# Kernel tuning notes

Hardware: AMD Instinct MI355X
Metric: run time of the kernel (lower is better)

Reference implementation:

```python
import jax, jax.numpy as jnp
import numpy as np

N = 100000   # nodes
E = 3200000  # directed edges
IN = 128     # in_channels
H = 16       # hidden_channels
OUT = 2      # out_channels
EPS = 1e-5   # BatchNorm eps


def setup_inputs() -> dict:
    key = jax.random.key(0)
    ks = jax.random.split(key, 16)
    x = jax.random.normal(ks[0], (N, IN), jnp.float32)
    edge_index = jax.random.randint(ks[1], (2, E), 0, N, jnp.int32)

    def lin(k, fan_in, fan_out):
        return jax.random.normal(k, (fan_in, fan_out), jnp.float32) / np.sqrt(fan_in)

    return {
        "x": x,
        "edge_index": edge_index,
        "W1": lin(ks[2], IN, H), "b1": jnp.zeros((H,), jnp.float32),
        "W2": lin(ks[3], H, H), "b2": jnp.zeros((H,), jnp.float32),
        "W3": lin(ks[4], H, H), "b3": jnp.zeros((H,), jnp.float32),
        "gamma1": jnp.ones((H,), jnp.float32), "beta1": jnp.zeros((H,), jnp.float32),
        "gamma2": jnp.ones((H,), jnp.float32), "beta2": jnp.zeros((H,), jnp.float32),
        "Wfc": lin(ks[5], H, OUT), "bfc": jnp.zeros((OUT,), jnp.float32),
    }


def reference(x, edge_index, W1, b1, W2, b2, W3, b3,
              gamma1, beta1, gamma2, beta2, Wfc, bfc):
    src, dst = edge_index[0], edge_index[1]
    # symmetric GCN normalization with self loops: deg includes +1 self loop
    deg = jax.ops.segment_sum(jnp.ones((E,), x.dtype), dst, num_segments=N) + 1.0
    dis = jax.lax.rsqrt(deg)                      # [N]
    norm = dis[src] * dis[dst]                    # [E]

    def gcn_conv(h, W, b):
        hw = h @ W                                # [N, F] dense transform
        msg = norm[:, None] * hw[src]             # gather + scale  [E, F]
        agg = jax.ops.segment_sum(msg, dst, num_segments=N)
        agg = agg + (dis * dis)[:, None] * hw     # self-loop contribution
        return agg + b

    def batch_norm(h, g, be):
        mu = h.mean(axis=0)
        var = h.var(axis=0)
        return (h - mu) * jax.lax.rsqrt(var + EPS) * g + be

    h = batch_norm(jax.nn.relu(gcn_conv(x, W1, b1)), gamma1, beta1)
    # dropout is identity in inference / deterministic reference
    h = batch_norm(jax.nn.relu(gcn_conv(h, W2, b2)), gamma2, beta2)
    h = gcn_conv(h, W3, b3)
    return jax.nn.log_softmax(h @ Wfc + bfc, axis=1)
```

## Files before the change

### kernel.cpp

```cpp
#include <hip/hip_runtime.h>
#include <hip/hip_fp16.h>

#define NN 100000
#define EE 3200000
#define INC 128
#define HC 16
#define BN_EPS 1e-5f

#define NPB 256
#define NBUCK ((NN + NPB - 1) / NPB)
#define CAPU 13440
#define BINSZ ((size_t)(NBUCK + 1) * CAPU)
#define BTILE 4096
#define BGRID ((EE + BTILE - 1) / BTILE)
#define SB_CAP 8960
#define GX32 (NN / 32)
#define GGRID (NN / 8)

#define XSTR 132

__device__ __forceinline__ __half2 bits_to_h2(int v) { __half2 h; *(int*)&h = v; return h; }
__device__ __forceinline__ int h2_to_bits(__half2 h) { return *(int*)&h; }


__global__ void init_all(int* __restrict__ bcursor, float* __restrict__ stats,
                         __half2* __restrict__ hws2) {
    int t = threadIdx.x;
    if (t < NBUCK) bcursor[t] = t * CAPU;
    if (t < 64) stats[t] = 0.f;
    if (t < 8) hws2[(size_t)NN * 8 + t] = __half2(__float2half2_rn(0.f));
}


__global__ __launch_bounds__(512) void build_gemm(const int* __restrict__ src,
                          const int* __restrict__ dst,
                          int* __restrict__ bcursor, unsigned* __restrict__ bin,
                          const float* __restrict__ x, const float* __restrict__ W1,
                          __half2* __restrict__ hw_raw) {
    __shared__ __align__(16) char smem[29312];
    int tid = threadIdx.x;
    if (blockIdx.x >= BGRID) {
        float* Ws = (float*)smem;
        float* xs = (float*)(smem + 8192);
        for (int i = tid; i < INC * HC; i += 512) Ws[i] = W1[i];
        int node0 = (blockIdx.x - BGRID) * 32;
        const float4* xsrc = (const float4*)(x + (size_t)node0 * INC);
        float4* xdst = (float4*)xs;
        for (int i = tid; i < 1024; i += 512) {
            int nl = i >> 5, k4 = i & 31;
            xdst[nl * 33 + k4] = xsrc[i];
        }
        __syncthreads();
        int c = tid & 15;
        int nl = tid >> 4;
        int node = node0 + nl;
        const float* xr = xs + nl * XSTR;
        float sum = 0.f;
#pragma unroll
        for (int k = 0; k < INC; ++k) sum += xr[k] * Ws[k * 16 + c];
        float other = __shfl_xor(sum, 1);
        if ((c & 1) == 0) hw_raw[node * 8 + (c >> 1)] = __floats2half2_rn(sum, other);
        return;
    }
    unsigned* stage = (unsigned*)smem;
    unsigned short* sbuck = (unsigned short*)(smem + 16384);
    int* hist  = (int*)(smem + 24576);
    int* loff  = (int*)(smem + 24576 + 1568);
    int* gbase = (int*)(smem + 24576 + 3136);
    int* wsum  = (int*)(smem + 24576 + 4704);
    int lane = tid & 63, wid = tid >> 6;
    for (int k = tid; k < NBUCK; k += 512) hist[k] = 0;
    __syncthreads();
    int e0 = blockIdx.x * BTILE;
    int cnt = min(BTILE, EE - e0);
    int n4 = cnt >> 2;
    const int4* d4 = (const int4*)(dst + e0);
    const int4* s4 = (const int4*)(src + e0);
    int4 dv0 = {0,0,0,0}, dv1 = {0,0,0,0}, sv0 = {0,0,0,0}, sv1 = {0,0,0,0};
    bool va0 = tid < n4, va1 = tid + 512 < n4;
    if (va0) {
        dv0 = d4[tid]; sv0 = s4[tid];
        atomicAdd(&hist[dv0.x >> 8], 1);
        atomicAdd(&hist[dv0.y >> 8], 1);
        atomicAdd(&hist[dv0.z >> 8], 1);
        atomicAdd(&hist[dv0.w >> 8], 1);
    }
    if (va1) {
        dv1 = d4[tid + 512]; sv1 = s4[tid + 512];
        atomicAdd(&hist[dv1.x >> 8], 1);
        atomicAdd(&hist[dv1.y >> 8], 1);
        atomicAdd(&hist[dv1.z >> 8], 1);
        atomicAdd(&hist[dv1.w >> 8], 1);
    }
    __syncthreads();
    int hv = (tid < NBUCK) ? hist[tid] : 0;
    int v = hv;
#pragma unroll
    for (int off = 1; off < 64; off <<= 1) {
        int t = __shfl_up(v, off);
        if (lane >= off) v += t;
    }
    if (lane == 63) wsum[wid] = v;
    __syncthreads();
    if (tid == 0) {
        int run = 0;
#pragma unroll
        for (int j = 0; j < 8; ++j) { int t = wsum[j]; wsum[j] = run; run += t; }
    }
    __syncthreads();
    int excl = v - hv + wsum[wid];
    if (tid < NBUCK) {
        loff[tid] = excl;
        if (hv) gbase[tid] = atomicAdd(&bcursor[tid], hv);
        hist[tid] = 0;
    }
    __syncthreads();
    {
        int d, s, k, p;
        if (va0) {
            d = dv0.x; s = sv0.x; k = d >> 8; p = loff[k] + atomicAdd(&hist[k], 1);
            stage[p] = ((unsigned)(d & 255) << 24) | (unsigned)s; sbuck[p] = (unsigned short)k;
            d = dv0.y; s = sv0.y; k = d >> 8; p = loff[k] + atomicAdd(&hist[k], 1);
            stage[p] = ((unsigned)(d & 255) << 24) | (unsigned)s; sbuck[p] = (unsigned short)k;
            d = dv0.z; s = sv0.z; k = d >> 8; p = loff[k] + atomicAdd(&hist[k], 1);
            stage[p] = ((unsigned)(d & 255) << 24) | (unsigned)s; sbuck[p] = (unsigned short)k;
            d = dv0.w; s = sv0.w; k = d >> 8; p = loff[k] + atomicAdd(&hist[k], 1);
            stage[p] = ((unsigned)(d & 255) << 24) | (unsigned)s; sbuck[p] = (unsigned short)k;
        }
        if (va1) {
            d = dv1.x; s = sv1.x; k = d >> 8; p = loff[k] + atomicAdd(&hist[k], 1);
            stage[p] = ((unsigned)(d & 255) << 24) | (unsigned)s; sbuck[p] = (unsigned short)k;
            d = dv1.y; s = sv1.y; k = d >> 8; p = loff[k] + atomicAdd(&hist[k], 1);
            stage[p] = ((unsigned)(d & 255) << 24) | (unsigned)s; sbuck[p] = (unsigned short)k;
            d = dv1.z; s = sv1.z; k = d >> 8; p = loff[k] + atomicAdd(&hist[k], 1);
            stage[p] = ((unsigned)(d & 255) << 24) | (unsigned)s; sbuck[p] = (unsigned short)k;
            d = dv1.w; s = sv1.w; k = d >> 8; p = loff[k] + atomicAdd(&hist[k], 1);
            stage[p] = ((unsigned)(d & 255) << 24) | (unsigned)s; sbuck[p] = (unsigned short)k;
        }
    }
    __syncthreads();
    for (int i = tid; i < cnt; i += 512) {
        int k = sbuck[i];
        int idx = gbase[k] + (i - loff[k]);
        if (idx < k * CAPU + SB_CAP) bin[idx] = stage[i];
    }
}


__global__ __launch_bounds__(512) void sort_bucket(const int* __restrict__ bcursor,
                            unsigned* __restrict__ bin,
                            unsigned* __restrict__ rowpack, float* __restrict__ dis,
                            const __half2* __restrict__ hw_raw, __half2* __restrict__ hws2) {
    __shared__ unsigned stg[SB_CAP];
    __shared__ int cnt[NPB], pos[NPB], sc[NPB];
    __shared__ int ptot_tot;
    int tid = threadIdx.x;
    for (int k = tid; k < NPB; k += 512) cnt[k] = 0;
    __syncthreads();
    int b = blockIdx.x;
    int beg = b * CAPU;
    int n = min(bcursor[b] - beg, SB_CAP);
    for (int i = tid; i < n; i += 512) {
        unsigned u = bin[beg + i];
        stg[i] = u;
        atomicAdd(&cnt[u >> 24], 1);
    }
    __syncthreads();
    int node = b * NPB + tid;
    int tot = 0, ptot = 0;
    if (tid < NPB) {
        tot = cnt[tid] + ((node < NN) ? 1 : 0);
        ptot = ((tot + 47) / 48) * 48;
        sc[tid] = ptot;
    }
    __syncthreads();
    for (int off = 1; off < NPB; off <<= 1) {
        int t = 0;
        if (tid < NPB && tid >= off) t = sc[tid - off];
        __syncthreads();
        if (tid < NPB) sc[tid] += t;
        __syncthreads();
    }
    int lo = 0;
    if (tid < NPB) {
        lo = sc[tid] - ptot;
        pos[tid] = lo + ((node < NN) ? 1 : 0);
        if (tid == NPB - 1) ptot_tot = sc[tid];
        if (node < NN) {
            rowpack[node] = ((unsigned)min(tot, 511) << 23) | (unsigned)(beg + lo);
            float dv = rsqrtf((float)tot);
            dis[node] = dv;
            __half2 d2 = __float2half2_rn(dv);
            const int4* hr = (const int4*)(hw_raw + (size_t)node * 8);
            int4 a = hr[0], bq = hr[1];
            __half2* ha = (__half2*)&a; __half2* hb = (__half2*)&bq;
#pragma unroll
            for (int j = 0; j < 4; ++j) { ha[j] = __hmul2(ha[j], d2); hb[j] = __hmul2(hb[j], d2); }
            int4* hw = (int4*)(hws2 + (size_t)node * 8);
            hw[0] = a; hw[1] = bq;
        }
    }
    __syncthreads();
    unsigned padv = (unsigned)NN << 5;
    int fillN = ptot_tot;
    for (int i = tid; i < fillN; i += 512) bin[beg + i] = padv;
    __syncthreads();
    if (tid < NPB && node < NN) bin[beg + lo] = (unsigned)node << 5;
    for (int i = tid; i < n; i += 512) {
        unsigned u = stg[i];
        int nl = u >> 24;
        int p = atomicAdd(&pos[nl], 1);
        bin[beg + p] = (u & 0xFFFFFFu) << 5;
    }
}


__global__ void gemm_bn_h_w(const float* __restrict__ agg, const float* __restrict__ stats,
                            const float* __restrict__ gamma, const float* __restrict__ beta,
                            const float* __restrict__ W, const float* __restrict__ dis,
                            __half2* __restrict__ hws2) {
    __shared__ float Ws[HC * HC];
    __shared__ float sc[HC], sf[HC];
    int tid = threadIdx.x;
    if (tid < HC * HC) Ws[tid] = W[tid];
    if (tid < HC) {
        const float invN = 1.0f / NN;
        float mu = stats[tid] * invN;
        float var = stats[16 + tid] * invN - mu * mu;
        float rs = rsqrtf(var + BN_EPS);
        sc[tid] = gamma[tid] * rs;
        sf[tid] = beta[tid] - mu * gamma[tid] * rs;
    }
    __syncthreads();
    int i = blockIdx.x * 256 + tid;
    if (i >= NN * HC) return;
    int n = i >> 4, c = i & 15;
    const float4* ar = (const float4*)(agg + n * HC);
    float sum = 0.f;
#pragma unroll
    for (int q = 0; q < 4; ++q) {
        float4 v = ar[q];
        int k = q * 4;
        float h0 = v.x * sc[k + 0] + sf[k + 0];
        float h1 = v.y * sc[k + 1] + sf[k + 1];
        float h2 = v.z * sc[k + 2] + sf[k + 2];
        float h3 = v.w * sc[k + 3] + sf[k + 3];
        sum += h0 * Ws[(k + 0) * 16 + c] + h1 * Ws[(k + 1) * 16 + c]
             + h2 * Ws[(k + 2) * 16 + c] + h3 * Ws[(k + 3) * 16 + c];
    }
    sum *= dis[n];
    float other = __shfl_xor(sum, 1);
    if ((c & 1) == 0) hws2[n * 8 + (c >> 1)] = __floats2half2_rn(sum, other);
}


__global__ __launch_bounds__(512) void gcn_gather(const unsigned* __restrict__ rowpack,
                           const unsigned* __restrict__ bin,
                           const __half2* __restrict__ hws2,
                           const float* __restrict__ b, float* __restrict__ agg,
                           float* __restrict__ partials) {
    __shared__ float acc[32];
    int tid = threadIdx.x;
    if (tid < 32) acc[tid] = 0.f;
    __syncthreads();
    int lane = tid & 63;
    int node = blockIdx.x * 8 + (tid >> 6);
    int cq = lane & 3;
    int slot = lane >> 2;
    unsigned rp = rowpack[node];
    int beg = (int)(rp & 0x7FFFFFu);
    int tot = (int)(rp >> 23);
    const char* hbase = (const char*)hws2;
    int e0 = beg + slot;
    unsigned v0 = bin[e0], v1 = bin[e0 + 16], v2 = bin[e0 + 32];
    int2 h0 = *(const int2*)(hbase + (size_t)v0 + cq * 8);
    int2 h1 = *(const int2*)(hbase + (size_t)v1 + cq * 8);
    int2 h2 = *(const int2*)(hbase + (size_t)v2 + cq * 8);
    __half2 accA = __hadd2(__hadd2(bits_to_h2(h0.x), bits_to_h2(h1.x)), bits_to_h2(h2.x));
    __half2 accB = __hadd2(__hadd2(bits_to_h2(h0.y), bits_to_h2(h1.y)), bits_to_h2(h2.y));
    for (int off = 48; off < tot; off += 48) {
        unsigned w0 = bin[e0 + off], w1 = bin[e0 + off + 16], w2 = bin[e0 + off + 32];
        int2 g0 = *(const int2*)(hbase + (size_t)w0 + cq * 8);
        int2 g1 = *(const int2*)(hbase + (size_t)w1 + cq * 8);
        int2 g2 = *(const int2*)(hbase + (size_t)w2 + cq * 8);
        accA = __hadd2(accA, __hadd2(__hadd2(bits_to_h2(g0.x), bits_to_h2(g1.x)), bits_to_h2(g2.x)));
        accB = __hadd2(accB, __hadd2(__hadd2(bits_to_h2(g0.y), bits_to_h2(g1.y)), bits_to_h2(g2.y)));
    }
    int ia = h2_to_bits(accA), ib = h2_to_bits(accB);
#pragma unroll
    for (int d = 4; d < 64; d <<= 1) {
        int oa = __shfl_xor(ia, d), ob = __shfl_xor(ib, d);
        accA = __hadd2(accA, bits_to_h2(oa));
        accB = __hadd2(accB, bits_to_h2(ob));
        ia = h2_to_bits(accA); ib = h2_to_bits(accB);
    }
    if (slot == 0) {
        float d = rsqrtf((float)tot);
        float2 sa = __half22float2(accA), sb = __half22float2(accB);
        float t0 = fmaxf(d * sa.x + b[4 * cq + 0], 0.f);
        float t1 = fmaxf(d * sa.y + b[4 * cq + 1], 0.f);
        float t2 = fmaxf(d * sb.x + b[4 * cq + 2], 0.f);
        float t3 = fmaxf(d * sb.y + b[4 * cq + 3], 0.f);
        float4 r; r.x = t0; r.y = t1; r.z = t2; r.w = t3;
        ((float4*)agg)[node * 4 + cq] = r;
        atomicAdd(&acc[4 * cq + 0], t0);
        atomicAdd(&acc[4 * cq + 1], t1);
        atomicAdd(&acc[4 * cq + 2], t2);
        atomicAdd(&acc[4 * cq + 3], t3);
        atomicAdd(&acc[16 + 4 * cq + 0], t0 * t0);
        atomicAdd(&acc[16 + 4 * cq + 1], t1 * t1);
        atomicAdd(&acc[16 + 4 * cq + 2], t2 * t2);
        atomicAdd(&acc[16 + 4 * cq + 3], t3 * t3);
    }
    __syncthreads();
    if (tid < 32) partials[(size_t)blockIdx.x * 32 + tid] = acc[tid];
}


__global__ void reduce_stats(const float* __restrict__ partials, float* __restrict__ stats) {
    int tid = threadIdx.x;
    const int total = GGRID * 32;
    float a = 0.f;
    int i0 = blockIdx.x * 256 + tid;
    for (int i = i0; i < total; i += gridDim.x * 256) a += partials[i];
    __shared__ float acc[32];
    if (tid < 32) acc[tid] = 0.f;
    __syncthreads();
    atomicAdd(&acc[i0 & 31], a);
    __syncthreads();
    if (tid < 32) atomicAdd(&stats[tid], acc[tid]);
}


__global__ __launch_bounds__(512) void gather_fc(const unsigned* __restrict__ rowpack,
                          const unsigned* __restrict__ bin,
                          const __half2* __restrict__ hws2,
                          const float* __restrict__ b, const float* __restrict__ Wfc,
                          const float* __restrict__ bfc, float* __restrict__ out) {
    int tid = threadIdx.x;
    int lane = tid & 63;
    int node = blockIdx.x * 8 + (tid >> 6);
    int cq = lane & 3;
    int slot = lane >> 2;
    unsigned rp = rowpack[node];
    int beg = (int)(rp & 0x7FFFFFu);
    int tot = (int)(rp >> 23);
    const char* hbase = (const char*)hws2;
    int e0 = beg + slot;
    unsigned v0 = bin[e0], v1 = bin[e0 + 16], v2 = bin[e0 + 32];
    int2 h0 = *(const int2*)(hbase + (size_t)v0 + cq * 8);
    int2 h1 = *(const int2*)(hbase + (size_t)v1 + cq * 8);
    int2 h2 = *(const int2*)(hbase + (size_t)v2 + cq * 8);
    __half2 accA = __hadd2(__hadd2(bits_to_h2(h0.x), bits_to_h2(h1.x)), bits_to_h2(h2.x));
    __half2 accB = __hadd2(__hadd2(bits_to_h2(h0.y), bits_to_h2(h1.y)), bits_to_h2(h2.y));
    for (int off = 48; off < tot; off += 48) {
        unsigned w0 = bin[e0 + off], w1 = bin[e0 + off + 16], w2 = bin[e0 + off + 32];
        int2 g0 = *(const int2*)(hbase + (size_t)w0 + cq * 8);
        int2 g1 = *(const int2*)(hbase + (size_t)w1 + cq * 8);
        int2 g2 = *(const int2*)(hbase + (size_t)w2 + cq * 8);
        accA = __hadd2(accA, __hadd2(__hadd2(bits_to_h2(g0.x), bits_to_h2(g1.x)), bits_to_h2(g2.x)));
        accB = __hadd2(accB, __hadd2(__hadd2(bits_to_h2(g0.y), bits_to_h2(g1.y)), bits_to_h2(g2.y)));
    }
    int ia = h2_to_bits(accA), ib = h2_to_bits(accB);
#pragma unroll
    for (int d = 4; d < 64; d <<= 1) {
        int oa = __shfl_xor(ia, d), ob = __shfl_xor(ib, d);
        accA = __hadd2(accA, bits_to_h2(oa));
        accB = __hadd2(accB, bits_to_h2(ob));
        ia = h2_to_bits(accA); ib = h2_to_bits(accB);
    }
    float z0 = 0.f, z1 = 0.f;
    if (slot == 0) {
        float d = rsqrtf((float)tot);
        float2 sa = __half22float2(accA), sb = __half22float2(accB);
        float v0f = d * sa.x + b[4 * cq + 0];
        float v1f = d * sa.y + b[4 * cq + 1];
        float v2f = d * sb.x + b[4 * cq + 2];
        float v3f = d * sb.y + b[4 * cq + 3];
        int k = 4 * cq;
        z0 = v0f * Wfc[(k + 0) * 2 + 0] + v1f * Wfc[(k + 1) * 2 + 0]
           + v2f * Wfc[(k + 2) * 2 + 0] + v3f * Wfc[(k + 3) * 2 + 0];
        z1 = v0f * Wfc[(k + 0) * 2 + 1] + v1f * Wfc[(k + 1) * 2 + 1]
           + v2f * Wfc[(k + 2) * 2 + 1] + v3f * Wfc[(k + 3) * 2 + 1];
    }
    z0 += __shfl_xor(z0, 1); z1 += __shfl_xor(z1, 1);
    z0 += __shfl_xor(z0, 2); z1 += __shfl_xor(z1, 2);
    if (lane == 0) {
        z0 += bfc[0]; z1 += bfc[1];
        float m = fmaxf(z0, z1);
        float lse = m + logf(expf(z0 - m) + expf(z1 - m));
        out[node * 2 + 0] = z0 - lse;
        out[node * 2 + 1] = z1 - lse;
    }
}


extern "C" void kernel_launch(void* const* d_in, const int* in_sizes, int n_in,
                              void* d_out, int out_size, void* d_ws, size_t ws_size,
                              hipStream_t stream) {
    const float* x    = (const float*)d_in[0];
    const int*   ei   = (const int*)d_in[1];
    const int*   src  = ei;
    const int*   dstp = ei + EE;
    const float* W1   = (const float*)d_in[2];
    const float* b1   = (const float*)d_in[3];
    const float* W2   = (const float*)d_in[4];
    const float* b2   = (const float*)d_in[5];
    const float* W3   = (const float*)d_in[6];
    const float* b3   = (const float*)d_in[7];
    const float* g1   = (const float*)d_in[8];
    const float* be1  = (const float*)d_in[9];
    const float* g2   = (const float*)d_in[10];
    const float* be2  = (const float*)d_in[11];
    const float* Wfc  = (const float*)d_in[12];
    const float* bfc  = (const float*)d_in[13];
    float* out = (float*)d_out;

    char* p = (char*)d_ws;
    unsigned* bin   = (unsigned*)p;             p += BINSZ * 4;
    __half2* hws2   = (__half2*)p;              p += (size_t)(NN + 1) * HC * 2;
    __half2* hw_raw = (__half2*)p;              p += (size_t)NN * HC * 2;
    float*  agg     = (float*)p;                p += (size_t)NN * HC * 4;
    float*  dis     = (float*)p;                p += (size_t)NN * 4;
    unsigned* rowpack=(unsigned*)p;             p += (size_t)NN * 4;
    float*  partials= (float*)p;                p += (size_t)GGRID * 32 * 4;
    int*    bcursor = (int*)p;                  p += NBUCK * 4;
    float*  stats1  = (float*)p;                p += 32 * 4;
    float*  stats2  = (float*)p;                p += 32 * 4;

    const int TB = 256;
    const int gNH = (NN * HC + TB - 1) / TB;

    init_all<<<1, 512, 0, stream>>>(bcursor, stats1, hws2);
    build_gemm<<<BGRID + GX32, 512, 0, stream>>>(src, dstp, bcursor, bin, x, W1, hw_raw);
    sort_bucket<<<NBUCK, 512, 0, stream>>>(bcursor, bin, rowpack, dis, hw_raw, hws2);

    gcn_gather<<<GGRID, 512, 0, stream>>>(rowpack, bin, hws2, b1, agg, partials);
    reduce_stats<<<64, 256, 0, stream>>>(partials, stats1);

    gemm_bn_h_w<<<gNH, TB, 0, stream>>>(agg, stats1, g1, be1, W2, dis, hws2);
    gcn_gather<<<GGRID, 512, 0, stream>>>(rowpack, bin, hws2, b2, agg, partials);
    reduce_stats<<<64, 256, 0, stream>>>(partials, stats2);

    gemm_bn_h_w<<<gNH, TB, 0, stream>>>(agg, stats2, g2, be2, W3, dis, hws2);
    gather_fc<<<GGRID, 512, 0, stream>>>(rowpack, bin, hws2, b3, Wfc, bfc, out);
}
```

Baseline: 232.2 us.

## Scatter edges directly to global bins, dropping the LDS staging pass, and double the tile

The bucketing pass no longer stages edges in shared memory in sorted order before a coalesced copy-out. Each edge is now written straight to its global bin slot, found from the per-bucket global base plus a local atomic counter. The edge tile per block goes from 4096 to 8192, so there are half as many blocks and fewer global cursor atomics per bucket. This removes one LDS round trip and a barrier, but the global writes become scattered rather than contiguous runs, and each thread holds more registers.

```diff
diff --git a/kernel.cpp b/kernel.cpp
--- a/kernel.cpp
+++ b/kernel.cpp
@@ -11,7 +11,7 @@
 #define NBUCK ((NN + NPB - 1) / NPB)
 #define CAPU 13440
 #define BINSZ ((size_t)(NBUCK + 1) * CAPU)
-#define BTILE 4096
+#define BTILE 8192
 #define BGRID ((EE + BTILE - 1) / BTILE)
 #define SB_CAP 8960
 #define GX32 (NN / 32)
@@ -37,7 +37,7 @@
                           int* __restrict__ bcursor, unsigned* __restrict__ bin,
                           const float* __restrict__ x, const float* __restrict__ W1,
                           __half2* __restrict__ hw_raw) {
-    __shared__ __align__(16) char smem[29312];
+    __shared__ __align__(16) char smem[25792];
     int tid = threadIdx.x;
     if (blockIdx.x >= BGRID) {
         float* Ws = (float*)smem;
@@ -62,12 +62,10 @@
         if ((c & 1) == 0) hw_raw[node * 8 + (c >> 1)] = __floats2half2_rn(sum, other);
         return;
     }
-    unsigned* stage = (unsigned*)smem;
-    unsigned short* sbuck = (unsigned short*)(smem + 16384);
-    int* hist  = (int*)(smem + 24576);
-    int* loff  = (int*)(smem + 24576 + 1568);
-    int* gbase = (int*)(smem + 24576 + 3136);
-    int* wsum  = (int*)(smem + 24576 + 4704);
+    int* hist  = (int*)smem;
+    int* loff  = (int*)(smem + 1568);
+    int* gbase = (int*)(smem + 3136);
+    int* wsum  = (int*)(smem + 4704);
     int lane = tid & 63, wid = tid >> 6;
     for (int k = tid; k < NBUCK; k += 512) hist[k] = 0;
     __syncthreads();
@@ -76,21 +74,17 @@
     int n4 = cnt >> 2;
     const int4* d4 = (const int4*)(dst + e0);
     const int4* s4 = (const int4*)(src + e0);
-    int4 dv0 = {0,0,0,0}, dv1 = {0,0,0,0}, sv0 = {0,0,0,0}, sv1 = {0,0,0,0};
-    bool va0 = tid < n4, va1 = tid + 512 < n4;
-    if (va0) {
-        dv0 = d4[tid]; sv0 = s4[tid];
-        atomicAdd(&hist[dv0.x >> 8], 1);
-        atomicAdd(&hist[dv0.y >> 8], 1);
-        atomicAdd(&hist[dv0.z >> 8], 1);
-        atomicAdd(&hist[dv0.w >> 8], 1);
-    }
-    if (va1) {
-        dv1 = d4[tid + 512]; sv1 = s4[tid + 512];
-        atomicAdd(&hist[dv1.x >> 8], 1);
-        atomicAdd(&hist[dv1.y >> 8], 1);
-        atomicAdd(&hist[dv1.z >> 8], 1);
-        atomicAdd(&hist[dv1.w >> 8], 1);
+    int4 dvr[4], svr[4];
+#pragma unroll
+    for (int j = 0; j < 4; ++j) {
+        int idx = tid + j * 512;
+        if (idx < n4) {
+            dvr[j] = d4[idx]; svr[j] = s4[idx];
+            atomicAdd(&hist[dvr[j].x >> 8], 1);
+            atomicAdd(&hist[dvr[j].y >> 8], 1);
+            atomicAdd(&hist[dvr[j].z >> 8], 1);
+            atomicAdd(&hist[dvr[j].w >> 8], 1);
+        }
     }
     __syncthreads();
     int hv = (tid < NBUCK) ? hist[tid] : 0;
@@ -108,41 +102,26 @@
         for (int j = 0; j < 8; ++j) { int t = wsum[j]; wsum[j] = run; run += t; }
     }
     __syncthreads();
-    int excl = v - hv + wsum[wid];
     if (tid < NBUCK) {
-        loff[tid] = excl;
-        if (hv) gbase[tid] = atomicAdd(&bcursor[tid], hv);
+        if (hv) gbase[tid] = atomicAdd(&bcursor[tid], hv) - 0;
         hist[tid] = 0;
     }
-    __syncthreads();
-    {
-        int d, s, k, p;
-        if (va0) {
-            d = dv0.x; s = sv0.x; k = d >> 8; p = loff[k] + atomicAdd(&hist[k], 1);
-            stage[p] = ((unsigned)(d & 255) << 24) | (unsigned)s; sbuck[p] = (unsigned short)k;
-            d = dv0.y; s = sv0.y; k = d >> 8; p = loff[k] + atomicAdd(&hist[k], 1);
-            stage[p] = ((unsigned)(d & 255) << 24) | (unsigned)s; sbuck[p] = (unsigned short)k;
-            d = dv0.z; s = sv0.z; k = d >> 8; p = loff[k] + atomicAdd(&hist[k], 1);
-            stage[p] = ((unsigned)(d & 255) << 24) | (unsigned)s; sbuck[p] = (unsigned short)k;
-            d = dv0.w; s = sv0.w; k = d >> 8; p = loff[k] + atomicAdd(&hist[k], 1);
-            stage[p] = ((unsigned)(d & 255) << 24) | (unsigned)s; sbuck[p] = (unsigned short)k;
+    (void)loff; (void)v;
+    __syncthreads();
+#pragma unroll
+    for (int j = 0; j < 4; ++j) {
+        int idx = tid + j * 512;
+        if (idx < n4) {
+            int d, s, k, p;
+            d = dvr[j].x; s = svr[j].x; k = d >> 8; p = gbase[k] + atomicAdd(&hist[k], 1);
+            if (p < k * CAPU + SB_CAP) bin[p] = ((unsigned)(d & 255) << 24) | (unsigned)s;
+            d = dvr[j].y; s = svr[j].y; k = d >> 8; p = gbase[k] + atomicAdd(&hist[k], 1);
+            if (p < k * CAPU + SB_CAP) bin[p] = ((unsigned)(d & 255) << 24) | (unsigned)s;
+            d = dvr[j].z; s = svr[j].z; k = d >> 8; p = gbase[k] + atomicAdd(&hist[k], 1);
+            if (p < k * CAPU + SB_CAP) bin[p] = ((unsigned)(d & 255) << 24) | (unsigned)s;
+            d = dvr[j].w; s = svr[j].w; k = d >> 8; p = gbase[k] + atomicAdd(&hist[k], 1);
+            if (p < k * CAPU + SB_CAP) bin[p] = ((unsigned)(d & 255) << 24) | (unsigned)s;
         }
-        if (va1) {
-            d = dv1.x; s = sv1.x; k = d >> 8; p = loff[k] + atomicAdd(&hist[k], 1);
-            stage[p] = ((unsigned)(d & 255) << 24) | (unsigned)s; sbuck[p] = (unsigned short)k;
-            d = dv1.y; s = sv1.y; k = d >> 8; p = loff[k] + atomicAdd(&hist[k], 1);
-            stage[p] = ((unsigned)(d & 255) << 24) | (unsigned)s; sbuck[p] = (unsigned short)k;
-            d = dv1.z; s = sv1.z; k = d >> 8; p = loff[k] + atomicAdd(&hist[k], 1);
-            stage[p] = ((unsigned)(d & 255) << 24) | (unsigned)s; sbuck[p] = (unsigned short)k;
-            d = dv1.w; s = sv1.w; k = d >> 8; p = loff[k] + atomicAdd(&hist[k], 1);
-            stage[p] = ((unsigned)(d & 255) << 24) | (unsigned)s; sbuck[p] = (unsigned short)k;
-        }
-    }
-    __syncthreads();
-    for (int i = tid; i < cnt; i += 512) {
-        int k = sbuck[i];
-        int idx = gbase[k] + (i - loff[k]);
-        if (idx < k * CAPU + SB_CAP) bin[idx] = stage[i];
     }
 }
 
```

Measured after the change: 227.2 us (median of 2 runs). 2.1% less time.
